# Optimization experiments

Hardware: AMD Instinct MI355X
Metric: run time of the kernel (lower is better)

The kernel has to match this reference:

```python
import jax
import jax.numpy as jnp
import numpy as np
from jax import lax

KSIZE = 3
C = 32


def _conv3x3(x, w):
    # NCHW input, OIHW weight, stride 1, padding 1 (matches nn.Conv2d(padding=1))
    return lax.conv_general_dilated(
        x, w, window_strides=(1, 1), padding=((1, 1), (1, 1)),
        dimension_numbers=("NCHW", "OIHW", "NCHW"))


def setup_inputs() -> dict:
    key = jax.random.key(0)
    k1, k2, k3 = jax.random.split(key, 3)
    N, H, W = 2, 64, 64
    x = jax.random.normal(k1, (N, C, H, W), dtype=jnp.float32)
    # conv1: C -> C, 3x3; PyTorch default init scale ~ 1/sqrt(fan_in)
    conv1_w = jax.random.normal(k2, (C, C, 3, 3), dtype=jnp.float32) * (1.0 / np.sqrt(C * 9))
    # conv2: C -> C*C*9, 3x3
    conv2_w = jax.random.normal(k3, (C * C * KSIZE * KSIZE, C, 3, 3), dtype=jnp.float32) * (1.0 / np.sqrt(C * 9))
    return {"x": x, "conv1_w": conv1_w, "conv2_w": conv2_w}


def reference(x, conv1_w, conv2_w):
    N, _, H, W = x.shape
    # kernel-generation branch: conv -> relu -> conv -> tanh
    h = jax.nn.relu(_conv3x3(x, conv1_w))
    rst = _conv3x3(h, conv2_w)  # [N, C*C*9, H, W]
    weight = jnp.tanh(rst.reshape(N, C, C, H, W, KSIZE, KSIZE))
    # non-uniform conv apply: per-pixel CxC 3x3 kernel, pad=1
    xp = jnp.pad(x, ((0, 0), (0, 0), (1, 1), (1, 1)))
    # patches[n, ci, h, w, kh, kw] = xp[n, ci, h+kh, w+kw]
    patches = jnp.stack(
        [xp[:, :, kh:kh + H, kw:kw + W] for kh in range(KSIZE) for kw in range(KSIZE)],
        axis=-1).reshape(N, C, H, W, KSIZE, KSIZE)
    out = jnp.einsum("noihwkl,nihwkl->nohw", weight, patches)
    return out
```

## Files before the change

kernel.cpp:

```cpp
#include <hip/hip_runtime.h>

typedef unsigned int uint;
typedef unsigned short ushort_t;

#define CN 32
#define HW 4096
#define KDIM 288
#define PDIM 8192
#define NB 2

typedef __attribute__((ext_vector_type(8))) short bf16x8;
typedef __attribute__((ext_vector_type(4))) float f32x4;

static __device__ __forceinline__ ushort_t f2bf(float f) {
    uint u = __float_as_uint(f);
    uint r = (u + 0x7fffu + ((u >> 16) & 1u)) >> 16;
    return (ushort_t)r;
}

static __device__ __forceinline__ void gl_lds16(const void* g, void* l) {
    __builtin_amdgcn_global_load_lds(
        (const __attribute__((address_space(1))) unsigned int*)g,
        (__attribute__((address_space(3))) unsigned int*)l, 16, 0, 0);
}

static __device__ __forceinline__ float fast_tanh(float v) {
    float e = __expf(2.0f * v);
    return 1.0f - 2.0f * __builtin_amdgcn_rcpf(e + 1.0f);
}


__global__ __launch_bounds__(256) void conv1_relu(
    const float* __restrict__ x, const float* __restrict__ w1,
    float* __restrict__ hout)
{
    __shared__ float w1s[KDIM];
    int bid = blockIdx.x;
    int c = (bid >> 2) & 31;
    int n = bid >> 7;
    for (int j = threadIdx.x; j < KDIM; j += 256) w1s[j] = w1[c * KDIM + j];
    __syncthreads();

    int idx = bid * 256 + threadIdx.x;
    int ws0 = (idx & 15) * 4;
    int hh  = (idx >> 4) & 63;

    float acc0 = 0.f, acc1 = 0.f, acc2 = 0.f, acc3 = 0.f;
    for (int ci = 0; ci < CN; ci++) {
        const float* xp = x + (((size_t)(n * CN + ci)) << 12);
        #pragma unroll
        for (int kh = 0; kh < 3; kh++) {
            int y = hh + kh - 1;
            if ((unsigned)y >= 64u) continue;
            const float* row = xp + (y << 6);
            float4 v = *(const float4*)(row + ws0);
            float left  = (ws0 > 0)  ? row[ws0 - 1] : 0.f;
            float right = (ws0 < 60) ? row[ws0 + 4] : 0.f;
            float rb[6] = {left, v.x, v.y, v.z, v.w, right};
            const float* wp = &w1s[ci * 9 + kh * 3];
            #pragma unroll
            for (int kw = 0; kw < 3; kw++) {
                float wgt = wp[kw];
                acc0 = fmaf(wgt, rb[0 + kw], acc0);
                acc1 = fmaf(wgt, rb[1 + kw], acc1);
                acc2 = fmaf(wgt, rb[2 + kw], acc2);
                acc3 = fmaf(wgt, rb[3 + kw], acc3);
            }
        }
    }
    float4 o = make_float4(fmaxf(acc0, 0.f), fmaxf(acc1, 0.f),
                           fmaxf(acc2, 0.f), fmaxf(acc3, 0.f));
    *(float4*)(hout + (((size_t)(n * CN + c)) << 12) + (hh << 6) + ws0) = o;
}

__global__ __launch_bounds__(256) void w2_to_bf16_perm(
    const float* __restrict__ in, ushort_t* __restrict__ out_bf,
    float4* __restrict__ out_zero)
{
    int idx = blockIdx.x * 256 + threadIdx.x;
    if (idx < 65536)
        out_zero[idx] = make_float4(0.f, 0.f, 0.f, 0.f);
    int row = idx / 36;
    int cw  = idx - row * 36;
    int g = cw >> 2, s = cw & 3;
    const float* base = in + (size_t)row * KDIM + g * 32;
    float4 lo = *(const float4*)(base + s * 4);
    float4 hi = *(const float4*)(base + 16 + s * 4);
    alignas(16) ushort_t o[8] = {f2bf(lo.x), f2bf(lo.y), f2bf(lo.z), f2bf(lo.w),
                                 f2bf(hi.x), f2bf(hi.y), f2bf(hi.z), f2bf(hi.w)};
    *(uint4*)(out_bf + (size_t)idx * 8) = *(const uint4*)o;
}

__global__ __launch_bounds__(256) void im2col_bf16_perm(
    const float* __restrict__ h, ushort_t* __restrict__ Bm)
{
    int idx = blockIdx.x * 256 + threadIdx.x;
    int p  = idx / 36;
    int cw = idx - p * 36;
    int g = cw >> 2, s = cw & 3;
    int n  = p >> 12;
    int sp = p & 4095;
    int hh = sp >> 6;
    int w  = sp & 63;
    const float* hn = h + (((size_t)n * CN) << 12);
    alignas(16) ushort_t o[8];
    #pragma unroll
    for (int j = 0; j < 8; j++) {
        int ko = (j < 4) ? (s * 4 + j) : (12 + s * 4 + j);
        int k  = g * 32 + ko;
        int ci = (k * 57) >> 9;
        int kk = k - ci * 9;
        int kh = (kk * 11) >> 5;
        int kw = kk - kh * 3;
        int y  = hh + kh - 1;
        int xw = w + kw - 1;
        float v = 0.f;
        if ((unsigned)y < 64u && (unsigned)xw < 64u)
            v = hn[((size_t)ci << 12) + (y << 6) + xw];
        o[j] = f2bf(v);
    }
    *(uint4*)(Bm + (size_t)idx * 8) = *(const uint4*)o;
}

__global__ __launch_bounds__(256, 4) void fused_gemm_apply(
    const ushort_t* __restrict__ A, const ushort_t* __restrict__ B,
    const float* __restrict__ x, float* __restrict__ out)
{
    __shared__ ushort_t AL[2][128 * 32];
    __shared__ ushort_t BL[2][128 * 32];
    __shared__ float vred[4][128];

    int tid = threadIdx.x;
    int bid = blockIdx.x;
    int sb  = (bid & 7) * 576 + (bid >> 3);
    int tw  = sb % 288;
    int cg  = (sb / 288) & 7;
    int n   = sb / 2304;

    int lane = tid & 63, wv = tid >> 6;
    int wm = wv >> 1, wn = wv & 1;
    int i16 = lane & 15, kg = lane >> 4;

    int T0 = tw * 128;
    int c8 = T0 >> 12;
    int q0 = T0 & 4095;

    int c_0 = tid, c_1 = 256 + tid;
    int row0 = c_0 >> 2, row1 = c_1 >> 2;
    int k8_0 = (((c_0 & 3) ^ ((c_0 >> 3) & 3)) << 3);
    int k8_1 = (((c_1 & 3) ^ ((c_1 >> 3) & 3)) << 3);
    const ushort_t* srcA0 = A +
        (size_t)((cg * 4 + (row0 >> 5)) * KDIM + (row0 & 31) * 9 + c8) * KDIM + k8_0;
    const ushort_t* srcA1 = A +
        (size_t)((cg * 4 + (row1 >> 5)) * KDIM + (row1 & 31) * 9 + c8) * KDIM + k8_1;
    const ushort_t* srcB0 = B + (size_t)((n << 12) + q0 + row0) * KDIM + k8_0;
    const ushort_t* srcB1 = B + (size_t)((n << 12) + q0 + row1) * KDIM + k8_1;
    int dst0 = wv * 512, dst1 = 2048 + wv * 512;

    f32x4 acc[4][4] = {};

    gl_lds16(srcA0, &AL[0][dst0]);
    gl_lds16(srcA1, &AL[0][dst1]);
    gl_lds16(srcB0, &BL[0][dst0]);
    gl_lds16(srcB1, &BL[0][dst1]);

    #pragma unroll
    for (int ks = 0; ks < 9; ks++) {
        int cur = ks & 1;
        if (ks < 8) {
            int k0 = (ks + 1) * 32;
            gl_lds16(srcA0 + k0, &AL[cur ^ 1][dst0]);
            gl_lds16(srcA1 + k0, &AL[cur ^ 1][dst1]);
            gl_lds16(srcB0 + k0, &BL[cur ^ 1][dst0]);
            gl_lds16(srcB1 + k0, &BL[cur ^ 1][dst1]);
            __builtin_amdgcn_sched_barrier(0);
            asm volatile("s_waitcnt vmcnt(4)" ::: "memory");
        } else {
            __builtin_amdgcn_sched_barrier(0);
            asm volatile("s_waitcnt vmcnt(0)" ::: "memory");
        }
        __builtin_amdgcn_sched_barrier(0);
        __builtin_amdgcn_s_barrier();
        __builtin_amdgcn_sched_barrier(0);

        bf16x8 af[4], bfr[4];
        #pragma unroll
        for (int mf = 0; mf < 4; mf++) {
            int row = wm * 64 + mf * 16 + i16;
            af[mf] = *(const bf16x8*)
                &AL[cur][row * 32 + ((kg ^ ((row >> 1) & 3)) << 3)];
        }
        #pragma unroll
        for (int nf = 0; nf < 4; nf++) {
            int row = wn * 64 + nf * 16 + i16;
            bfr[nf] = *(const bf16x8*)
                &BL[cur][row * 32 + ((kg ^ ((row >> 1) & 3)) << 3)];
        }
        #pragma unroll
        for (int mf = 0; mf < 4; mf++)
            #pragma unroll
            for (int nf = 0; nf < 4; nf++)
                acc[mf][nf] = __builtin_amdgcn_mfma_f32_16x16x32_bf16(
                    af[mf], bfr[nf], acc[mf][nf], 0, 0, 0);

        __builtin_amdgcn_sched_barrier(0);
        asm volatile("s_waitcnt lgkmcnt(0)" ::: "memory");
        __builtin_amdgcn_sched_barrier(0);
        __builtin_amdgcn_s_barrier();
        __builtin_amdgcn_sched_barrier(0);
    }

    const float* xn = x + (((size_t)n * CN) << 12);
    #pragma unroll
    for (int nf = 0; nf < 4; nf++) {
        int t  = T0 + wn * 64 + nf * 16 + i16;
        uint sp = ((uint)t * 58255u) >> 19;
        int kk = t - (int)sp * 9;
        int kh = (kk * 11) >> 5;
        int kw = kk - kh * 3;
        int y  = (int)(sp >> 6) + kh - 1;
        int xw = (int)(sp & 63) + kw - 1;
        bool ok = ((unsigned)y < 64u) && ((unsigned)xw < 64u);
        int poff = (y << 6) + xw;
        float xa[4], xb[4];
        #pragma unroll
        for (int r = 0; r < 4; r++) {
            int cia = kg * 4 + r;
            xa[r] = ok ? xn[((size_t)cia << 12) + poff] : 0.f;
            xb[r] = ok ? xn[((size_t)(cia + 16) << 12) + poff] : 0.f;
        }
        float s0 = 0.f, s1 = 0.f;
        #pragma unroll
        for (int r = 0; r < 4; r++) {
            s0 = fmaf(fast_tanh(acc[0][nf][r]), xa[r], s0);
            s0 = fmaf(fast_tanh(acc[1][nf][r]), xb[r], s0);
            s1 = fmaf(fast_tanh(acc[2][nf][r]), xa[r], s1);
            s1 = fmaf(fast_tanh(acc[3][nf][r]), xb[r], s1);
        }
        s0 += __shfl_xor(s0, 16); s0 += __shfl_xor(s0, 32);
        s1 += __shfl_xor(s1, 16); s1 += __shfl_xor(s1, 32);
        if (kg == 0) {
            vred[2 * wm + 0][wn * 64 + nf * 16 + i16] = s0;
            vred[2 * wm + 1][wn * 64 + nf * 16 + i16] = s1;
        }
    }
    __syncthreads();

    if (tid < 64) {
        int g  = tid >> 4, bi = tid & 15;
        uint spA = ((uint)T0 * 58255u) >> 19;
        int sp = (int)spA + bi;
        int lo = sp * 9;     if (lo < T0) lo = T0;
        int hi = sp * 9 + 9; if (hi > T0 + 128) hi = T0 + 128;
        if (lo < hi) {
            float s = 0.f;
            for (int t = lo; t < hi; t++) s += vred[g][t - T0];
            atomicAdd(&out[(((size_t)n * CN + cg * 4 + g) << 12) + sp], s);
        }
    }
}

extern "C" void kernel_launch(void* const* d_in, const int* in_sizes, int n_in,
                              void* d_out, int out_size, void* d_ws, size_t ws_size,
                              hipStream_t stream) {
    const float* x  = (const float*)d_in[0];
    const float* w1 = (const float*)d_in[1];
    const float* w2 = (const float*)d_in[2];
    float* out = (float*)d_out;
    char* ws = (char*)d_ws;

    float*    hbuf  = (float*)ws;
    ushort_t* Bm_bf = (ushort_t*)(ws + 1048576u);
    ushort_t* A_bf  = (ushort_t*)(ws + 5767168u);

    hipLaunchKernelGGL(conv1_relu, dim3(256), dim3(256), 0, stream, x, w1, hbuf);
    hipLaunchKernelGGL(w2_to_bf16_perm, dim3(1296), dim3(256), 0, stream,
                       w2, A_bf, (float4*)out);
    hipLaunchKernelGGL(im2col_bf16_perm, dim3(1152), dim3(256), 0,
                       stream, hbuf, Bm_bf);
    hipLaunchKernelGGL(fused_gemm_apply, dim3(4608), dim3(256), 0, stream,
                       A_bf, Bm_bf, x, out);
}
```

Before: 118.4 us.

## Widen GEMM tile to 128x256 with 8 waves and merge prep kernels

Each GEMM block now covers 256 columns of the t dimension instead of 128, using 512 threads (8 waves). The A tile is shared across twice the B columns, which halves A traffic per output and halves the block count. The conv1 and weight-conversion kernels are also merged into one launch to save a kernel boundary. The cost is more LDS per block and possibly lower occupancy, and launch_bounds(512,4) may limit registers.

```diff
diff --git a/kernel.cpp b/kernel.cpp
--- a/kernel.cpp
+++ b/kernel.cpp
@@ -30,65 +30,63 @@
 }
 
 
-__global__ __launch_bounds__(256) void conv1_relu(
+__global__ __launch_bounds__(256) void prep_kernel(
     const float* __restrict__ x, const float* __restrict__ w1,
-    float* __restrict__ hout)
+    const float* __restrict__ w2, float* __restrict__ hout,
+    ushort_t* __restrict__ A_bf, float4* __restrict__ out_zero)
 {
     __shared__ float w1s[KDIM];
-    int bid = blockIdx.x;
-    int c = (bid >> 2) & 31;
-    int n = bid >> 7;
-    for (int j = threadIdx.x; j < KDIM; j += 256) w1s[j] = w1[c * KDIM + j];
-    __syncthreads();
-
-    int idx = bid * 256 + threadIdx.x;
-    int ws0 = (idx & 15) * 4;
-    int hh  = (idx >> 4) & 63;
-
-    float acc0 = 0.f, acc1 = 0.f, acc2 = 0.f, acc3 = 0.f;
-    for (int ci = 0; ci < CN; ci++) {
-        const float* xp = x + (((size_t)(n * CN + ci)) << 12);
-        #pragma unroll
-        for (int kh = 0; kh < 3; kh++) {
-            int y = hh + kh - 1;
-            if ((unsigned)y >= 64u) continue;
-            const float* row = xp + (y << 6);
-            float4 v = *(const float4*)(row + ws0);
-            float left  = (ws0 > 0)  ? row[ws0 - 1] : 0.f;
-            float right = (ws0 < 60) ? row[ws0 + 4] : 0.f;
-            float rb[6] = {left, v.x, v.y, v.z, v.w, right};
-            const float* wp = &w1s[ci * 9 + kh * 3];
+    int bb = blockIdx.x;
+    if (bb < 256) {
+        int c = (bb >> 2) & 31;
+        int n = bb >> 7;
+        for (int j = threadIdx.x; j < KDIM; j += 256) w1s[j] = w1[c * KDIM + j];
+        __syncthreads();
+
+        int idx = bb * 256 + threadIdx.x;
+        int ws0 = (idx & 15) * 4;
+        int hh  = (idx >> 4) & 63;
+
+        float acc0 = 0.f, acc1 = 0.f, acc2 = 0.f, acc3 = 0.f;
+        for (int ci = 0; ci < CN; ci++) {
+            const float* xp = x + (((size_t)(n * CN + ci)) << 12);
             #pragma unroll
-            for (int kw = 0; kw < 3; kw++) {
-                float wgt = wp[kw];
-                acc0 = fmaf(wgt, rb[0 + kw], acc0);
-                acc1 = fmaf(wgt, rb[1 + kw], acc1);
-                acc2 = fmaf(wgt, rb[2 + kw], acc2);
-                acc3 = fmaf(wgt, rb[3 + kw], acc3);
+            for (int kh = 0; kh < 3; kh++) {
+                int y = hh + kh - 1;
+                if ((unsigned)y >= 64u) continue;
+                const float* row = xp + (y << 6);
+                float4 v = *(const float4*)(row + ws0);
+                float left  = (ws0 > 0)  ? row[ws0 - 1] : 0.f;
+                float right = (ws0 < 60) ? row[ws0 + 4] : 0.f;
+                float rb[6] = {left, v.x, v.y, v.z, v.w, right};
+                const float* wp = &w1s[ci * 9 + kh * 3];
+                #pragma unroll
+                for (int kw = 0; kw < 3; kw++) {
+                    float wgt = wp[kw];
+                    acc0 = fmaf(wgt, rb[0 + kw], acc0);
+                    acc1 = fmaf(wgt, rb[1 + kw], acc1);
+                    acc2 = fmaf(wgt, rb[2 + kw], acc2);
+                    acc3 = fmaf(wgt, rb[3 + kw], acc3);
+                }
             }
         }
-    }
-    float4 o = make_float4(fmaxf(acc0, 0.f), fmaxf(acc1, 0.f),
-                           fmaxf(acc2, 0.f), fmaxf(acc3, 0.f));
-    *(float4*)(hout + (((size_t)(n * CN + c)) << 12) + (hh << 6) + ws0) = o;
-}
-
-__global__ __launch_bounds__(256) void w2_to_bf16_perm(
-    const float* __restrict__ in, ushort_t* __restrict__ out_bf,
-    float4* __restrict__ out_zero)
-{
-    int idx = blockIdx.x * 256 + threadIdx.x;
-    if (idx < 65536)
-        out_zero[idx] = make_float4(0.f, 0.f, 0.f, 0.f);
-    int row = idx / 36;
-    int cw  = idx - row * 36;
-    int g = cw >> 2, s = cw & 3;
-    const float* base = in + (size_t)row * KDIM + g * 32;
-    float4 lo = *(const float4*)(base + s * 4);
-    float4 hi = *(const float4*)(base + 16 + s * 4);
-    alignas(16) ushort_t o[8] = {f2bf(lo.x), f2bf(lo.y), f2bf(lo.z), f2bf(lo.w),
-                                 f2bf(hi.x), f2bf(hi.y), f2bf(hi.z), f2bf(hi.w)};
-    *(uint4*)(out_bf + (size_t)idx * 8) = *(const uint4*)o;
+        float4 o = make_float4(fmaxf(acc0, 0.f), fmaxf(acc1, 0.f),
+                               fmaxf(acc2, 0.f), fmaxf(acc3, 0.f));
+        *(float4*)(hout + (((size_t)(n * CN + c)) << 12) + (hh << 6) + ws0) = o;
+    } else {
+        int idx = (bb - 256) * 256 + threadIdx.x;
+        if (idx < 65536)
+            out_zero[idx] = make_float4(0.f, 0.f, 0.f, 0.f);
+        int row = idx / 36;
+        int cw  = idx - row * 36;
+        int g = cw >> 2, s = cw & 3;
+        const float* base = w2 + (size_t)row * KDIM + g * 32;
+        float4 lo = *(const float4*)(base + s * 4);
+        float4 hi = *(const float4*)(base + 16 + s * 4);
+        alignas(16) ushort_t o[8] = {f2bf(lo.x), f2bf(lo.y), f2bf(lo.z), f2bf(lo.w),
+                                     f2bf(hi.x), f2bf(hi.y), f2bf(hi.z), f2bf(hi.w)};
+        *(uint4*)(A_bf + (size_t)idx * 8) = *(const uint4*)o;
+    }
 }
 
 __global__ __launch_bounds__(256) void im2col_bf16_perm(
@@ -122,59 +120,59 @@
     *(uint4*)(Bm + (size_t)idx * 8) = *(const uint4*)o;
 }
 
-__global__ __launch_bounds__(256, 4) void fused_gemm_apply(
+__global__ __launch_bounds__(512, 4) void fused_gemm_apply(
     const ushort_t* __restrict__ A, const ushort_t* __restrict__ B,
     const float* __restrict__ x, float* __restrict__ out)
 {
     __shared__ ushort_t AL[2][128 * 32];
-    __shared__ ushort_t BL[2][128 * 32];
-    __shared__ float vred[4][128];
+    __shared__ ushort_t BL[2][256 * 32];
+    __shared__ float vred[4][256];
 
     int tid = threadIdx.x;
     int bid = blockIdx.x;
-    int sb  = (bid & 7) * 576 + (bid >> 3);
-    int tw  = sb % 288;
-    int cg  = (sb / 288) & 7;
-    int n   = sb / 2304;
+    int sb  = (bid & 7) * 288 + (bid >> 3);
+    int tw  = sb % 144;
+    int cg  = (sb / 144) & 7;
+    int n   = sb / 1152;
 
     int lane = tid & 63, wv = tid >> 6;
-    int wm = wv >> 1, wn = wv & 1;
+    int wm = wv >> 2, wt = wv & 3;
     int i16 = lane & 15, kg = lane >> 4;
 
-    int T0 = tw * 128;
+    int T0 = tw * 256;
     int c8 = T0 >> 12;
     int q0 = T0 & 4095;
 
-    int c_0 = tid, c_1 = 256 + tid;
-    int row0 = c_0 >> 2, row1 = c_1 >> 2;
-    int k8_0 = (((c_0 & 3) ^ ((c_0 >> 3) & 3)) << 3);
-    int k8_1 = (((c_1 & 3) ^ ((c_1 >> 3) & 3)) << 3);
-    const ushort_t* srcA0 = A +
-        (size_t)((cg * 4 + (row0 >> 5)) * KDIM + (row0 & 31) * 9 + c8) * KDIM + k8_0;
-    const ushort_t* srcA1 = A +
-        (size_t)((cg * 4 + (row1 >> 5)) * KDIM + (row1 & 31) * 9 + c8) * KDIM + k8_1;
-    const ushort_t* srcB0 = B + (size_t)((n << 12) + q0 + row0) * KDIM + k8_0;
-    const ushort_t* srcB1 = B + (size_t)((n << 12) + q0 + row1) * KDIM + k8_1;
-    int dst0 = wv * 512, dst1 = 2048 + wv * 512;
+    int cA = tid;
+    int rA = cA >> 2;
+    int k8A = (((cA & 3) ^ ((cA >> 3) & 3)) << 3);
+    const ushort_t* srcA = A +
+        (size_t)((cg * 4 + (rA >> 5)) * KDIM + (rA & 31) * 9 + c8) * KDIM + k8A;
+    int cB0 = tid, cB1 = 512 + tid;
+    int rB0 = cB0 >> 2, rB1 = cB1 >> 2;
+    int k8B0 = (((cB0 & 3) ^ ((cB0 >> 3) & 3)) << 3);
+    int k8B1 = (((cB1 & 3) ^ ((cB1 >> 3) & 3)) << 3);
+    const ushort_t* srcB0 = B + (size_t)((n << 12) + q0 + rB0) * KDIM + k8B0;
+    const ushort_t* srcB1 = B + (size_t)((n << 12) + q0 + rB1) * KDIM + k8B1;
+    int dstA = wv * 512;
+    int dstB0 = wv * 512, dstB1 = 4096 + wv * 512;
 
     f32x4 acc[4][4] = {};
 
-    gl_lds16(srcA0, &AL[0][dst0]);
-    gl_lds16(srcA1, &AL[0][dst1]);
-    gl_lds16(srcB0, &BL[0][dst0]);
-    gl_lds16(srcB1, &BL[0][dst1]);
+    gl_lds16(srcA,  &AL[0][dstA]);
+    gl_lds16(srcB0, &BL[0][dstB0]);
+    gl_lds16(srcB1, &BL[0][dstB1]);
 
     #pragma unroll
     for (int ks = 0; ks < 9; ks++) {
         int cur = ks & 1;
         if (ks < 8) {
             int k0 = (ks + 1) * 32;
-            gl_lds16(srcA0 + k0, &AL[cur ^ 1][dst0]);
-            gl_lds16(srcA1 + k0, &AL[cur ^ 1][dst1]);
-            gl_lds16(srcB0 + k0, &BL[cur ^ 1][dst0]);
-            gl_lds16(srcB1 + k0, &BL[cur ^ 1][dst1]);
+            gl_lds16(srcA + k0,  &AL[cur ^ 1][dstA]);
+            gl_lds16(srcB0 + k0, &BL[cur ^ 1][dstB0]);
+            gl_lds16(srcB1 + k0, &BL[cur ^ 1][dstB1]);
             __builtin_amdgcn_sched_barrier(0);
-            asm volatile("s_waitcnt vmcnt(4)" ::: "memory");
+            asm volatile("s_waitcnt vmcnt(3)" ::: "memory");
         } else {
             __builtin_amdgcn_sched_barrier(0);
             asm volatile("s_waitcnt vmcnt(0)" ::: "memory");
@@ -192,7 +190,7 @@
         }
         #pragma unroll
         for (int nf = 0; nf < 4; nf++) {
-            int row = wn * 64 + nf * 16 + i16;
+            int row = wt * 64 + nf * 16 + i16;
             bfr[nf] = *(const bf16x8*)
                 &BL[cur][row * 32 + ((kg ^ ((row >> 1) & 3)) << 3)];
         }
@@ -213,7 +211,7 @@
     const float* xn = x + (((size_t)n * CN) << 12);
     #pragma unroll
     for (int nf = 0; nf < 4; nf++) {
-        int t  = T0 + wn * 64 + nf * 16 + i16;
+        int t  = T0 + wt * 64 + nf * 16 + i16;
         uint sp = ((uint)t * 58255u) >> 19;
         int kk = t - (int)sp * 9;
         int kh = (kk * 11) >> 5;
@@ -240,18 +238,18 @@
         s0 += __shfl_xor(s0, 16); s0 += __shfl_xor(s0, 32);
         s1 += __shfl_xor(s1, 16); s1 += __shfl_xor(s1, 32);
         if (kg == 0) {
-            vred[2 * wm + 0][wn * 64 + nf * 16 + i16] = s0;
-            vred[2 * wm + 1][wn * 64 + nf * 16 + i16] = s1;
+            vred[2 * wm + 0][wt * 64 + nf * 16 + i16] = s0;
+            vred[2 * wm + 1][wt * 64 + nf * 16 + i16] = s1;
         }
     }
     __syncthreads();
 
-    if (tid < 64) {
-        int g  = tid >> 4, bi = tid & 15;
+    if (tid < 128) {
+        int g  = tid >> 5, bi = tid & 31;
         uint spA = ((uint)T0 * 58255u) >> 19;
         int sp = (int)spA + bi;
         int lo = sp * 9;     if (lo < T0) lo = T0;
-        int hi = sp * 9 + 9; if (hi > T0 + 128) hi = T0 + 128;
+        int hi = sp * 9 + 9; if (hi > T0 + 256) hi = T0 + 256;
         if (lo < hi) {
             float s = 0.f;
             for (int t = lo; t < hi; t++) s += vred[g][t - T0];
@@ -273,11 +271,10 @@
     ushort_t* Bm_bf = (ushort_t*)(ws + 1048576u);
     ushort_t* A_bf  = (ushort_t*)(ws + 5767168u);
 
-    hipLaunchKernelGGL(conv1_relu, dim3(256), dim3(256), 0, stream, x, w1, hbuf);
-    hipLaunchKernelGGL(w2_to_bf16_perm, dim3(1296), dim3(256), 0, stream,
-                       w2, A_bf, (float4*)out);
+    hipLaunchKernelGGL(prep_kernel, dim3(1552), dim3(256), 0, stream,
+                       x, w1, w2, hbuf, A_bf, (float4*)out);
     hipLaunchKernelGGL(im2col_bf16_perm, dim3(1152), dim3(256), 0,
                        stream, hbuf, Bm_bf);
-    hipLaunchKernelGGL(fused_gemm_apply, dim3(4608), dim3(256), 0, stream,
+    hipLaunchKernelGGL(fused_gemm_apply, dim3(2304), dim3(512), 0, stream,
                        A_bf, Bm_bf, x, out);
 }
```

New measurement: 114.5 us. -3.3%, faster.

## Load GEMM fragments directly from global into registers and merge prep kernels

Applied to the files above, without the earlier changes.

The fused GEMM kernel no longer stages A and B tiles through LDS with global_load_lds double buffering and barriers. Each wave now loads its bf16 MFMA fragments straight from global memory into registers, with a two-set register ping-pong to prefetch the next K slice. The occupancy hint in launch bounds is dropped. The conv1 and weight-conversion kernels are also merged into one launch to save a kernel launch. The risks are that tiles shared between waves get reloaded redundantly through the cache, global loads are less coalesced, and register pressure rises.

```diff
diff --git a/kernel.cpp b/kernel.cpp
--- a/kernel.cpp
+++ b/kernel.cpp
@@ -18,77 +18,69 @@
     return (ushort_t)r;
 }
 
-static __device__ __forceinline__ void gl_lds16(const void* g, void* l) {
-    __builtin_amdgcn_global_load_lds(
-        (const __attribute__((address_space(1))) unsigned int*)g,
-        (__attribute__((address_space(3))) unsigned int*)l, 16, 0, 0);
-}
-
 static __device__ __forceinline__ float fast_tanh(float v) {
     float e = __expf(2.0f * v);
     return 1.0f - 2.0f * __builtin_amdgcn_rcpf(e + 1.0f);
 }
 
 
-__global__ __launch_bounds__(256) void conv1_relu(
+__global__ __launch_bounds__(256) void prep_kernel(
     const float* __restrict__ x, const float* __restrict__ w1,
-    float* __restrict__ hout)
+    const float* __restrict__ w2, float* __restrict__ hout,
+    ushort_t* __restrict__ A_bf, float4* __restrict__ out_zero)
 {
     __shared__ float w1s[KDIM];
-    int bid = blockIdx.x;
-    int c = (bid >> 2) & 31;
-    int n = bid >> 7;
-    for (int j = threadIdx.x; j < KDIM; j += 256) w1s[j] = w1[c * KDIM + j];
-    __syncthreads();
-
-    int idx = bid * 256 + threadIdx.x;
-    int ws0 = (idx & 15) * 4;
-    int hh  = (idx >> 4) & 63;
-
-    float acc0 = 0.f, acc1 = 0.f, acc2 = 0.f, acc3 = 0.f;
-    for (int ci = 0; ci < CN; ci++) {
-        const float* xp = x + (((size_t)(n * CN + ci)) << 12);
-        #pragma unroll
-        for (int kh = 0; kh < 3; kh++) {
-            int y = hh + kh - 1;
-            if ((unsigned)y >= 64u) continue;
-            const float* row = xp + (y << 6);
-            float4 v = *(const float4*)(row + ws0);
-            float left  = (ws0 > 0)  ? row[ws0 - 1] : 0.f;
-            float right = (ws0 < 60) ? row[ws0 + 4] : 0.f;
-            float rb[6] = {left, v.x, v.y, v.z, v.w, right};
-            const float* wp = &w1s[ci * 9 + kh * 3];
+    int bb = blockIdx.x;
+    if (bb < 256) {
+        int c = (bb >> 2) & 31;
+        int n = bb >> 7;
+        for (int j = threadIdx.x; j < KDIM; j += 256) w1s[j] = w1[c * KDIM + j];
+        __syncthreads();
+
+        int idx = bb * 256 + threadIdx.x;
+        int ws0 = (idx & 15) * 4;
+        int hh  = (idx >> 4) & 63;
+
+        float acc0 = 0.f, acc1 = 0.f, acc2 = 0.f, acc3 = 0.f;
+        for (int ci = 0; ci < CN; ci++) {
+            const float* xp = x + (((size_t)(n * CN + ci)) << 12);
             #pragma unroll
-            for (int kw = 0; kw < 3; kw++) {
-                float wgt = wp[kw];
-                acc0 = fmaf(wgt, rb[0 + kw], acc0);
-                acc1 = fmaf(wgt, rb[1 + kw], acc1);
-                acc2 = fmaf(wgt, rb[2 + kw], acc2);
-                acc3 = fmaf(wgt, rb[3 + kw], acc3);
+            for (int kh = 0; kh < 3; kh++) {
+                int y = hh + kh - 1;
+                if ((unsigned)y >= 64u) continue;
+                const float* row = xp + (y << 6);
+                float4 v = *(const float4*)(row + ws0);
+                float left  = (ws0 > 0)  ? row[ws0 - 1] : 0.f;
+                float right = (ws0 < 60) ? row[ws0 + 4] : 0.f;
+                float rb[6] = {left, v.x, v.y, v.z, v.w, right};
+                const float* wp = &w1s[ci * 9 + kh * 3];
+                #pragma unroll
+                for (int kw = 0; kw < 3; kw++) {
+                    float wgt = wp[kw];
+                    acc0 = fmaf(wgt, rb[0 + kw], acc0);
+                    acc1 = fmaf(wgt, rb[1 + kw], acc1);
+                    acc2 = fmaf(wgt, rb[2 + kw], acc2);
+                    acc3 = fmaf(wgt, rb[3 + kw], acc3);
+                }
             }
         }
-    }
-    float4 o = make_float4(fmaxf(acc0, 0.f), fmaxf(acc1, 0.f),
-                           fmaxf(acc2, 0.f), fmaxf(acc3, 0.f));
-    *(float4*)(hout + (((size_t)(n * CN + c)) << 12) + (hh << 6) + ws0) = o;
-}
-
-__global__ __launch_bounds__(256) void w2_to_bf16_perm(
-    const float* __restrict__ in, ushort_t* __restrict__ out_bf,
-    float4* __restrict__ out_zero)
-{
-    int idx = blockIdx.x * 256 + threadIdx.x;
-    if (idx < 65536)
-        out_zero[idx] = make_float4(0.f, 0.f, 0.f, 0.f);
-    int row = idx / 36;
-    int cw  = idx - row * 36;
-    int g = cw >> 2, s = cw & 3;
-    const float* base = in + (size_t)row * KDIM + g * 32;
-    float4 lo = *(const float4*)(base + s * 4);
-    float4 hi = *(const float4*)(base + 16 + s * 4);
-    alignas(16) ushort_t o[8] = {f2bf(lo.x), f2bf(lo.y), f2bf(lo.z), f2bf(lo.w),
-                                 f2bf(hi.x), f2bf(hi.y), f2bf(hi.z), f2bf(hi.w)};
-    *(uint4*)(out_bf + (size_t)idx * 8) = *(const uint4*)o;
+        float4 o = make_float4(fmaxf(acc0, 0.f), fmaxf(acc1, 0.f),
+                               fmaxf(acc2, 0.f), fmaxf(acc3, 0.f));
+        *(float4*)(hout + (((size_t)(n * CN + c)) << 12) + (hh << 6) + ws0) = o;
+    } else {
+        int idx = (bb - 256) * 256 + threadIdx.x;
+        if (idx < 65536)
+            out_zero[idx] = make_float4(0.f, 0.f, 0.f, 0.f);
+        int row = idx / 36;
+        int cw  = idx - row * 36;
+        int g = cw >> 2, s = cw & 3;
+        const float* base = w2 + (size_t)row * KDIM + g * 32;
+        float4 lo = *(const float4*)(base + s * 4);
+        float4 hi = *(const float4*)(base + 16 + s * 4);
+        alignas(16) ushort_t o[8] = {f2bf(lo.x), f2bf(lo.y), f2bf(lo.z), f2bf(lo.w),
+                                     f2bf(hi.x), f2bf(hi.y), f2bf(hi.z), f2bf(hi.w)};
+        *(uint4*)(A_bf + (size_t)idx * 8) = *(const uint4*)o;
+    }
 }
 
 __global__ __launch_bounds__(256) void im2col_bf16_perm(
@@ -122,12 +114,10 @@
     *(uint4*)(Bm + (size_t)idx * 8) = *(const uint4*)o;
 }
 
-__global__ __launch_bounds__(256, 4) void fused_gemm_apply(
+__global__ __launch_bounds__(256) void fused_gemm_apply(
     const ushort_t* __restrict__ A, const ushort_t* __restrict__ B,
     const float* __restrict__ x, float* __restrict__ out)
 {
-    __shared__ ushort_t AL[2][128 * 32];
-    __shared__ ushort_t BL[2][128 * 32];
     __shared__ float vred[4][128];
 
     int tid = threadIdx.x;
@@ -145,70 +135,66 @@
     int c8 = T0 >> 12;
     int q0 = T0 & 4095;
 
-    int c_0 = tid, c_1 = 256 + tid;
-    int row0 = c_0 >> 2, row1 = c_1 >> 2;
-    int k8_0 = (((c_0 & 3) ^ ((c_0 >> 3) & 3)) << 3);
-    int k8_1 = (((c_1 & 3) ^ ((c_1 >> 3) & 3)) << 3);
-    const ushort_t* srcA0 = A +
-        (size_t)((cg * 4 + (row0 >> 5)) * KDIM + (row0 & 31) * 9 + c8) * KDIM + k8_0;
-    const ushort_t* srcA1 = A +
-        (size_t)((cg * 4 + (row1 >> 5)) * KDIM + (row1 & 31) * 9 + c8) * KDIM + k8_1;
-    const ushort_t* srcB0 = B + (size_t)((n << 12) + q0 + row0) * KDIM + k8_0;
-    const ushort_t* srcB1 = B + (size_t)((n << 12) + q0 + row1) * KDIM + k8_1;
-    int dst0 = wv * 512, dst1 = 2048 + wv * 512;
+    const ushort_t *pA0, *pA1, *pA2, *pA3, *pB0, *pB1, *pB2, *pB3;
+    {
+        int r0 = wm * 64 + 0 * 16 + i16, r1 = wm * 64 + 1 * 16 + i16;
+        int r2 = wm * 64 + 2 * 16 + i16, r3 = wm * 64 + 3 * 16 + i16;
+        pA0 = A + (size_t)((cg * 4 + (r0 >> 5)) * KDIM + (r0 & 31) * 9 + c8) * KDIM + kg * 8;
+        pA1 = A + (size_t)((cg * 4 + (r1 >> 5)) * KDIM + (r1 & 31) * 9 + c8) * KDIM + kg * 8;
+        pA2 = A + (size_t)((cg * 4 + (r2 >> 5)) * KDIM + (r2 & 31) * 9 + c8) * KDIM + kg * 8;
+        pA3 = A + (size_t)((cg * 4 + (r3 >> 5)) * KDIM + (r3 & 31) * 9 + c8) * KDIM + kg * 8;
+        int b0 = (n << 12) + q0 + wn * 64 + 0 * 16 + i16;
+        int b1 = b0 + 16, b2 = b0 + 32, b3 = b0 + 48;
+        pB0 = B + (size_t)b0 * KDIM + kg * 8;
+        pB1 = B + (size_t)b1 * KDIM + kg * 8;
+        pB2 = B + (size_t)b2 * KDIM + kg * 8;
+        pB3 = B + (size_t)b3 * KDIM + kg * 8;
+    }
 
     f32x4 acc[4][4] = {};
-
-    gl_lds16(srcA0, &AL[0][dst0]);
-    gl_lds16(srcA1, &AL[0][dst1]);
-    gl_lds16(srcB0, &BL[0][dst0]);
-    gl_lds16(srcB1, &BL[0][dst1]);
-
-    #pragma unroll
-    for (int ks = 0; ks < 9; ks++) {
-        int cur = ks & 1;
-        if (ks < 8) {
-            int k0 = (ks + 1) * 32;
-            gl_lds16(srcA0 + k0, &AL[cur ^ 1][dst0]);
-            gl_lds16(srcA1 + k0, &AL[cur ^ 1][dst1]);
-            gl_lds16(srcB0 + k0, &BL[cur ^ 1][dst0]);
-            gl_lds16(srcB1 + k0, &BL[cur ^ 1][dst1]);
-            __builtin_amdgcn_sched_barrier(0);
-            asm volatile("s_waitcnt vmcnt(4)" ::: "memory");
-        } else {
-            __builtin_amdgcn_sched_barrier(0);
-            asm volatile("s_waitcnt vmcnt(0)" ::: "memory");
-        }
-        __builtin_amdgcn_sched_barrier(0);
-        __builtin_amdgcn_s_barrier();
-        __builtin_amdgcn_sched_barrier(0);
-
-        bf16x8 af[4], bfr[4];
-        #pragma unroll
-        for (int mf = 0; mf < 4; mf++) {
-            int row = wm * 64 + mf * 16 + i16;
-            af[mf] = *(const bf16x8*)
-                &AL[cur][row * 32 + ((kg ^ ((row >> 1) & 3)) << 3)];
-        }
-        #pragma unroll
-        for (int nf = 0; nf < 4; nf++) {
-            int row = wn * 64 + nf * 16 + i16;
-            bfr[nf] = *(const bf16x8*)
-                &BL[cur][row * 32 + ((kg ^ ((row >> 1) & 3)) << 3)];
-        }
-        #pragma unroll
-        for (int mf = 0; mf < 4; mf++)
-            #pragma unroll
-            for (int nf = 0; nf < 4; nf++)
-                acc[mf][nf] = __builtin_amdgcn_mfma_f32_16x16x32_bf16(
-                    af[mf], bfr[nf], acc[mf][nf], 0, 0, 0);
-
-        __builtin_amdgcn_sched_barrier(0);
-        asm volatile("s_waitcnt lgkmcnt(0)" ::: "memory");
-        __builtin_amdgcn_sched_barrier(0);
-        __builtin_amdgcn_s_barrier();
-        __builtin_amdgcn_sched_barrier(0);
-    }
+    bf16x8 a00, a01, a02, a03, b00, b01, b02, b03;
+    bf16x8 a10, a11, a12, a13, b10, b11, b12, b13;
+
+#define LDSET(AA0, AA1, AA2, AA3, BB0, BB1, BB2, BB3, OFS)            \
+    do { int _o = (OFS);                                              \
+        AA0 = *(const bf16x8*)(pA0 + _o); AA1 = *(const bf16x8*)(pA1 + _o); \
+        AA2 = *(const bf16x8*)(pA2 + _o); AA3 = *(const bf16x8*)(pA3 + _o); \
+        BB0 = *(const bf16x8*)(pB0 + _o); BB1 = *(const bf16x8*)(pB1 + _o); \
+        BB2 = *(const bf16x8*)(pB2 + _o); BB3 = *(const bf16x8*)(pB3 + _o); \
+    } while (0)
+
+#define MMSET(AA0, AA1, AA2, AA3, BB0, BB1, BB2, BB3)                 \
+    do {                                                              \
+        acc[0][0] = __builtin_amdgcn_mfma_f32_16x16x32_bf16(AA0, BB0, acc[0][0], 0, 0, 0); \
+        acc[0][1] = __builtin_amdgcn_mfma_f32_16x16x32_bf16(AA0, BB1, acc[0][1], 0, 0, 0); \
+        acc[0][2] = __builtin_amdgcn_mfma_f32_16x16x32_bf16(AA0, BB2, acc[0][2], 0, 0, 0); \
+        acc[0][3] = __builtin_amdgcn_mfma_f32_16x16x32_bf16(AA0, BB3, acc[0][3], 0, 0, 0); \
+        acc[1][0] = __builtin_amdgcn_mfma_f32_16x16x32_bf16(AA1, BB0, acc[1][0], 0, 0, 0); \
+        acc[1][1] = __builtin_amdgcn_mfma_f32_16x16x32_bf16(AA1, BB1, acc[1][1], 0, 0, 0); \
+        acc[1][2] = __builtin_amdgcn_mfma_f32_16x16x32_bf16(AA1, BB2, acc[1][2], 0, 0, 0); \
+        acc[1][3] = __builtin_amdgcn_mfma_f32_16x16x32_bf16(AA1, BB3, acc[1][3], 0, 0, 0); \
+        acc[2][0] = __builtin_amdgcn_mfma_f32_16x16x32_bf16(AA2, BB0, acc[2][0], 0, 0, 0); \
+        acc[2][1] = __builtin_amdgcn_mfma_f32_16x16x32_bf16(AA2, BB1, acc[2][1], 0, 0, 0); \
+        acc[2][2] = __builtin_amdgcn_mfma_f32_16x16x32_bf16(AA2, BB2, acc[2][2], 0, 0, 0); \
+        acc[2][3] = __builtin_amdgcn_mfma_f32_16x16x32_bf16(AA2, BB3, acc[2][3], 0, 0, 0); \
+        acc[3][0] = __builtin_amdgcn_mfma_f32_16x16x32_bf16(AA3, BB0, acc[3][0], 0, 0, 0); \
+        acc[3][1] = __builtin_amdgcn_mfma_f32_16x16x32_bf16(AA3, BB1, acc[3][1], 0, 0, 0); \
+        acc[3][2] = __builtin_amdgcn_mfma_f32_16x16x32_bf16(AA3, BB2, acc[3][2], 0, 0, 0); \
+        acc[3][3] = __builtin_amdgcn_mfma_f32_16x16x32_bf16(AA3, BB3, acc[3][3], 0, 0, 0); \
+    } while (0)
+
+    LDSET(a00, a01, a02, a03, b00, b01, b02, b03, 0);
+    #pragma unroll 1
+    for (int it = 0; it < 4; ++it) {
+        int ks = it * 2;
+        LDSET(a10, a11, a12, a13, b10, b11, b12, b13, (ks + 1) * 32);
+        MMSET(a00, a01, a02, a03, b00, b01, b02, b03);
+        LDSET(a00, a01, a02, a03, b00, b01, b02, b03, (ks + 2) * 32);
+        MMSET(a10, a11, a12, a13, b10, b11, b12, b13);
+    }
+    MMSET(a00, a01, a02, a03, b00, b01, b02, b03);
+#undef LDSET
+#undef MMSET
 
     const float* xn = x + (((size_t)n * CN) << 12);
     #pragma unroll
@@ -273,9 +259,8 @@
     ushort_t* Bm_bf = (ushort_t*)(ws + 1048576u);
     ushort_t* A_bf  = (ushort_t*)(ws + 5767168u);
 
-    hipLaunchKernelGGL(conv1_relu, dim3(256), dim3(256), 0, stream, x, w1, hbuf);
-    hipLaunchKernelGGL(w2_to_bf16_perm, dim3(1296), dim3(256), 0, stream,
-                       w2, A_bf, (float4*)out);
+    hipLaunchKernelGGL(prep_kernel, dim3(1552), dim3(256), 0, stream,
+                       x, w1, w2, hbuf, A_bf, (float4*)out);
     hipLaunchKernelGGL(im2col_bf16_perm, dim3(1152), dim3(256), 0,
                        stream, hbuf, Bm_bf);
     hipLaunchKernelGGL(fused_gemm_apply, dim3(4608), dim3(256), 0, stream,
```

Result: slower. 170.4 us (+43.9%).
